# Optimization experiments

Measured on AMD Instinct MI355X. Metric: run time of the kernel, lower is better.

The kernel has to match this reference:

```python
import jax, jax.numpy as jnp
import numpy as np

B, H, W, C, F = 32, 32, 32, 256, 64
K_NEIGH = 32  # L1 pixel-distance cutoff used for the static mask


def _distance_mask(h, w, k):
    # coords: [hw, 2] of (y, x); L1 pixel distances, normalized by max(h, w)
    ys, xs = jnp.meshgrid(jnp.arange(h), jnp.arange(w), indexing='ij')
    coords = jnp.stack([ys, xs], axis=-1).reshape(-1, 2).astype(jnp.float32)
    diff = jnp.abs(coords[:, None, :] - coords[None, :, :]).sum(-1)  # [hw, hw], == cdist p=1
    dist = diff / float(max(h, w))
    return jnp.where(diff <= k, dist, 0.0)


def setup_inputs() -> dict:
    key = jax.random.key(0)
    ks = jax.random.split(key, 7)
    return {
        'feature_map': jax.random.normal(ks[0], (B, H, W, C), dtype=jnp.float32),
        'emb_W': jax.random.normal(ks[1], (F, C), dtype=jnp.float32) * (1.0 / np.sqrt(C)),
        'emb_b': jax.random.normal(ks[2], (F,), dtype=jnp.float32) * 0.01,
        'attn_W': jax.random.normal(ks[3], (C, C), dtype=jnp.float32) * (1.0 / np.sqrt(C)),
        'attn_b': jax.random.normal(ks[4], (C,), dtype=jnp.float32) * 0.01,
        'thr_W': jax.random.normal(ks[5], (1, C), dtype=jnp.float32) * (1.0 / np.sqrt(C)),
        'thr_b': jax.random.normal(ks[6], (1,), dtype=jnp.float32) * 0.01,
        'layer': 0,
    }


def reference(feature_map, emb_W, emb_b, attn_W, attn_b, thr_W, thr_b, layer):
    b, h, w, c = feature_map.shape
    hw = h * w
    x = feature_map.reshape(b, hw, c)  # row-major (y, x) flatten, matches torch view

    # 1x1 conv -> per-pixel linear: instance embeddings [b, hw, F]
    emb = jnp.einsum('bnc,fc->bnf', x, emb_W) + emb_b

    # squared Euclidean pairwise distances (cdist p=2, then squared)
    sq = jnp.sum(emb * emb, axis=-1)  # [b, hw]
    d2 = jnp.maximum(sq[:, :, None] + sq[:, None, :]
                     - 2.0 * jnp.einsum('bnf,bmf->bnm', emb, emb), 0.0)

    mask = _distance_mask(h, w, K_NEIGH)  # [hw, hw] static buffer
    sim = jax.nn.softmax(jnp.exp(-d2) - (1.0 - mask), axis=-1)  # [b, hw, hw]

    # shortcut = attention_conv(feature_map): [b, hw, c]
    shortcut = jnp.einsum('bnc,dc->bnd', x, attn_W) + attn_b

    # per-pixel learned threshold: [b, hw]
    Tinst = (jnp.einsum('bnc,oc->bno', shortcut, thr_W) + thr_b)[..., 0]

    A = jax.nn.softmax(jnp.maximum(sim - Tinst[:, None, :], 0.0), axis=-1)

    # bmm: out[b, i, c] = sum_j shortcut[b, j, c] * A[b, i, j]
    attn_out = jnp.einsum('bjc,bij->bic', shortcut, A)

    res = (x + attn_out).reshape(b, h, w, c)
    return res
```

## Files before the change

kernel.cpp:

```cpp
#include <hip/hip_runtime.h>
#include <hip/hip_bf16.h>


typedef short bf16x8 __attribute__((ext_vector_type(8)));
typedef float f32x4 __attribute__((ext_vector_type(4)));

__device__ __forceinline__ unsigned short f2bf(float f) {
  unsigned u = __float_as_uint(f);
  u += 0x7fffu + ((u >> 16) & 1u);
  return (unsigned short)(u >> 16);
}
__device__ __forceinline__ float bf2f(unsigned short h) {
  return __uint_as_float(((unsigned)h) << 16);
}
__device__ __forceinline__ unsigned pack2(float a, float b) {
  return (unsigned)f2bf(a) | ((unsigned)f2bf(b) << 16);
}
__device__ __forceinline__ f32x4 mfma16(bf16x8 a, bf16x8 b, f32x4 c) {
  return __builtin_amdgcn_mfma_f32_16x16x32_bf16(a, b, c, 0, 0, 0);
}
__device__ __forceinline__ int iabs(int v) { return v < 0 ? -v : v; }
__device__ __forceinline__ void load_lds16(const void* g, void* l) {
  __builtin_amdgcn_global_load_lds(
      (const __attribute__((address_space(1))) unsigned int*)g,
      (__attribute__((address_space(3))) unsigned int*)l, 16, 0, 0);
}

__global__ __launch_bounds__(256) void k_emb(const float* __restrict__ x,
                                             const float* __restrict__ embW,
                                             const float* __restrict__ embB,
                                             unsigned short* __restrict__ embb,
                                             float* __restrict__ sq) {
  __shared__ unsigned short xs[64][40];
  __shared__ unsigned short ws[64][40];
  __shared__ float sqls[64];
  const int t = threadIdx.x;
  const int Mbase = blockIdx.x * 64;
  const int lane = t & 63, wave = t >> 6;
  const int wm = wave >> 1, wn = wave & 1;
  const int l15 = lane & 15, quad = lane >> 4;

  f32x4 acc[2][2] = {};
  for (int k0 = 0; k0 < 256; k0 += 32) {
    {
      int row = t >> 2, c0 = (t & 3) * 8;
      const float* src = x + (size_t)(Mbase + row) * 256 + k0 + c0;
      float4 a = *(const float4*)src;
      float4 b = *(const float4*)(src + 4);
      uint4 p; p.x = pack2(a.x, a.y); p.y = pack2(a.z, a.w);
      p.z = pack2(b.x, b.y); p.w = pack2(b.z, b.w);
      *(uint4*)&xs[row][c0] = p;
    }
    if (t < 64) {
      const float* wsrc = embW + (size_t)t * 256 + k0;
      for (int s = 0; s < 4; s++) {
        float4 a = *(const float4*)(wsrc + s * 8);
        float4 b = *(const float4*)(wsrc + s * 8 + 4);
        uint4 p; p.x = pack2(a.x, a.y); p.y = pack2(a.z, a.w);
        p.z = pack2(b.x, b.y); p.w = pack2(b.z, b.w);
        *(uint4*)&ws[t][s * 8] = p;
      }
    }
    __syncthreads();
    bf16x8 af[2], bfr[2];
    for (int rt = 0; rt < 2; rt++)
      af[rt] = *(const bf16x8*)&xs[wm * 32 + rt * 16 + l15][quad * 8];
    for (int ct = 0; ct < 2; ct++)
      bfr[ct] = *(const bf16x8*)&ws[wn * 32 + ct * 16 + l15][quad * 8];
    for (int rt = 0; rt < 2; rt++)
      for (int ct = 0; ct < 2; ct++)
        acc[rt][ct] = mfma16(af[rt], bfr[ct], acc[rt][ct]);
    __syncthreads();
  }

  if (t < 64) sqls[t] = 0.f;
  __syncthreads();
  float sp[2][4] = {};
  for (int rt = 0; rt < 2; rt++)
    for (int ct = 0; ct < 2; ct++) {
      int f = wn * 32 + ct * 16 + l15;
      float bias = embB[f];
      for (int r = 0; r < 4; r++) {
        float v = acc[rt][ct][r] + bias;
        unsigned short hb = f2bf(v);
        int rowl = wm * 32 + rt * 16 + quad * 4 + r;
        embb[(size_t)(Mbase + rowl) * 64 + f] = hb;
        float vf = bf2f(hb);
        sp[rt][r] += vf * vf;
      }
    }
  for (int m = 8; m >= 1; m >>= 1)
    for (int rt = 0; rt < 2; rt++)
      for (int r = 0; r < 4; r++)
        sp[rt][r] += __shfl_xor(sp[rt][r], m);
  if (l15 == 0)
    for (int rt = 0; rt < 2; rt++)
      for (int r = 0; r < 4; r++)
        atomicAdd(&sqls[wm * 32 + rt * 16 + quad * 4 + r], sp[rt][r]);
  __syncthreads();
  if (t < 64) sq[Mbase + t] = sqls[t];
}

__global__ __launch_bounds__(256) void k_shortcut(const float* __restrict__ x,
                                                  const float* __restrict__ attnW,
                                                  const float* __restrict__ attnB,
                                                  const float* __restrict__ thrW,
                                                  const float* __restrict__ thrB,
                                                  unsigned short* __restrict__ scT,
                                                  float* __restrict__ Tout) {
  __shared__ unsigned short xs[64][40];
  __shared__ unsigned short ws[256][40];
  __shared__ unsigned short St[256][72];
  const int t = threadIdx.x;
  const int Mbase = blockIdx.x * 64;
  const int lane = t & 63, wave = t >> 6;
  const int wm = wave >> 1, wn = wave & 1;
  const int l15 = lane & 15, quad = lane >> 4;

  f32x4 acc[2][8] = {};
  for (int k0 = 0; k0 < 256; k0 += 32) {
    {
      int row = t >> 2, c0 = (t & 3) * 8;
      const float* src = x + (size_t)(Mbase + row) * 256 + k0 + c0;
      float4 a = *(const float4*)src;
      float4 b = *(const float4*)(src + 4);
      uint4 p; p.x = pack2(a.x, a.y); p.y = pack2(a.z, a.w);
      p.z = pack2(b.x, b.y); p.w = pack2(b.z, b.w);
      *(uint4*)&xs[row][c0] = p;
    }
    {
      const float* wsrc = attnW + (size_t)t * 256 + k0;
      for (int s = 0; s < 4; s++) {
        float4 a = *(const float4*)(wsrc + s * 8);
        float4 b = *(const float4*)(wsrc + s * 8 + 4);
        uint4 p; p.x = pack2(a.x, a.y); p.y = pack2(a.z, a.w);
        p.z = pack2(b.x, b.y); p.w = pack2(b.z, b.w);
        *(uint4*)&ws[t][s * 8] = p;
      }
    }
    __syncthreads();
    bf16x8 af[2];
    for (int rt = 0; rt < 2; rt++)
      af[rt] = *(const bf16x8*)&xs[wm * 32 + rt * 16 + l15][quad * 8];
    for (int nt = 0; nt < 8; nt++) {
      bf16x8 bfr = *(const bf16x8*)&ws[wn * 128 + nt * 16 + l15][quad * 8];
      for (int rt = 0; rt < 2; rt++)
        acc[rt][nt] = mfma16(af[rt], bfr, acc[rt][nt]);
    }
    __syncthreads();
  }

  for (int rt = 0; rt < 2; rt++)
    for (int nt = 0; nt < 8; nt++) {
      int c = wn * 128 + nt * 16 + l15;
      float bias = attnB[c];
      for (int r = 0; r < 4; r++) {
        float v = acc[rt][nt][r] + bias;
        int j = wm * 32 + rt * 16 + quad * 4 + r;
        St[c][j] = f2bf(v);
      }
    }
  __syncthreads();
  const int b = Mbase >> 10, jbase = Mbase & 1023;
  {
    unsigned short* dst = scT + ((size_t)b * 256 + t) * 1024 + jbase;
    for (int s = 0; s < 8; s++)
      *(uint4*)(dst + s * 8) = *(const uint4*)&St[t][s * 8];
  }
  {
    float tp = 0.f;
    int j = t >> 2, cs = (t & 3) * 64;
    for (int c = 0; c < 64; c++)
      tp += bf2f(St[cs + c][j]) * thrW[cs + c];
    tp += __shfl_xor(tp, 1);
    tp += __shfl_xor(tp, 2);
    if ((t & 3) == 0) Tout[Mbase + j] = tp + thrB[0];
  }
}

__global__ __launch_bounds__(256) void k_scores(const unsigned short* __restrict__ embb,
                                                const float* __restrict__ sq,
                                                const float* __restrict__ T,
                                                unsigned short* __restrict__ U,
                                                float* __restrict__ Z) {
  __shared__ unsigned short E_lds[16 * 1040];
  __shared__ float rbuf[16];
  const int t = threadIdx.x, lane = t & 63, wave = t >> 6;
  const int b = blockIdx.x >> 6, rb = (blockIdx.x & 63) * 16;
  const int l15 = lane & 15, quad = lane >> 4;
  const unsigned short* eb = embb + (size_t)b * 1024 * 64;

  if (t < 16) rbuf[t] = 0.f;

  const int rowA = rb + l15;
  bf16x8 a0 = *(const bf16x8*)(eb + (size_t)rowA * 64 + quad * 8);
  bf16x8 a1 = *(const bf16x8*)(eb + (size_t)rowA * 64 + 32 + quad * 8);
  const int rloc = quad * 4;
  float sqi[4]; int yi[4], xi[4];
  for (int r = 0; r < 4; r++) {
    int rowg = rb + rloc + r;
    sqi[r] = sq[b * 1024 + rowg];
    yi[r] = rowg >> 5; xi[r] = rowg & 31;
  }
  const int jq = wave * 256;
  float rp[4] = {0.f, 0.f, 0.f, 0.f};
  for (int j0 = jq; j0 < jq + 256; j0 += 16) {
    const int jr = j0 + l15;
    bf16x8 b0 = *(const bf16x8*)(eb + (size_t)jr * 64 + quad * 8);
    bf16x8 b1 = *(const bf16x8*)(eb + (size_t)jr * 64 + 32 + quad * 8);
    f32x4 g = {0.f, 0.f, 0.f, 0.f};
    g = mfma16(a0, b0, g);
    g = mfma16(a1, b1, g);
    float sqj = sq[b * 1024 + jr];
    int yj = jr >> 5, xj = jr & 31;
    for (int r = 0; r < 4; r++) {
      float d2 = fmaxf(sqi[r] + sqj - 2.f * g[r], 0.f);
      int diff = iabs(yi[r] - yj) + iabs(xi[r] - xj);
      float m = (diff <= 32) ? (float)diff * (1.f / 32.f) : 0.f;
      float s = __expf(-d2) - 1.f + m;
      unsigned short h = f2bf(__expf(s));
      E_lds[(rloc + r) * 1040 + jr] = h;
      rp[r] += bf2f(h);
    }
  }
  for (int m = 8; m >= 1; m >>= 1)
    for (int r = 0; r < 4; r++)
      rp[r] += __shfl_xor(rp[r], m);
  __syncthreads();
  if (l15 == 0)
    for (int r = 0; r < 4; r++)
      atomicAdd(&rbuf[rloc + r], rp[r]);
  __syncthreads();

  const int prow = t >> 4, seg = t & 15;
  const float invR = 1.f / rbuf[prow];
  const float* Tb = T + b * 1024;
  unsigned short* ur = U + ((size_t)(b * 1024 + rb + prow)) * 1024;
  float z = 0.f;
  for (int c = 0; c < 8; c++) {
    int j = c * 128 + seg * 8;
    union { bf16x8 v; unsigned short s[8]; } ev;
    ev.v = *(const bf16x8*)&E_lds[prow * 1040 + j];
    float4 t0 = *(const float4*)(Tb + j);
    float4 t1 = *(const float4*)(Tb + j + 4);
    float tf[8] = {t0.x, t0.y, t0.z, t0.w, t1.x, t1.y, t1.z, t1.w};
    union { uint4 v; unsigned short s[8]; } uo;
    for (int k = 0; k < 8; k++) {
      float u = __expf(fmaxf(fmaf(bf2f(ev.s[k]), invR, -tf[k]), 0.f));
      unsigned short h = f2bf(u);
      uo.s[k] = h;
      z += bf2f(h);
    }
    *(uint4*)(ur + j) = uo.v;
  }
  z += __shfl_xor(z, 1);
  z += __shfl_xor(z, 2);
  z += __shfl_xor(z, 4);
  z += __shfl_xor(z, 8);
  if (seg == 0) Z[b * 1024 + rb + prow] = z;
}

__global__ __launch_bounds__(256) void k_out(const unsigned short* __restrict__ U,
                                             const float* __restrict__ Z,
                                             const unsigned short* __restrict__ scT,
                                             const float* __restrict__ x,
                                             float* __restrict__ out) {
  __shared__ unsigned short Ab[128 * 32];
  __shared__ unsigned short Bb[128 * 32];
  const int t = threadIdx.x, lane = t & 63, wave = t >> 6;
  const int wm = wave >> 1, wn = wave & 1;
  const int l15 = lane & 15, quad = lane >> 4;
  const int x8 = blockIdx.x & 7, s = blockIdx.x >> 3;
  const int b = x8 * 4 + (s >> 4), tile = s & 15;
  const int rb = (tile >> 1) * 128, cb = (tile & 1) * 128;

  const unsigned short* Ubase = U + (size_t)b * 1024 * 1024 + (size_t)rb * 1024;
  const unsigned short* Sbase = scT + (size_t)b * 256 * 1024 + (size_t)cb * 1024;

  int c0 = wave * 64 + lane;
  int c1 = c0 + 256;
  const int r0 = c0 >> 2, o0 = (c0 & 3) * 8;
  const int r1 = c1 >> 2, o1 = (c1 & 3) * 8;

  f32x4 acc[4][4] = {};
  for (int j0 = 0; j0 < 1024; j0 += 32) {
    load_lds16(Ubase + (size_t)r0 * 1024 + j0 + o0, Ab + c0 * 8);
    load_lds16(Ubase + (size_t)r1 * 1024 + j0 + o1, Ab + c1 * 8);
    load_lds16(Sbase + (size_t)r0 * 1024 + j0 + o0, Bb + c0 * 8);
    load_lds16(Sbase + (size_t)r1 * 1024 + j0 + o1, Bb + c1 * 8);
    __syncthreads();
    bf16x8 af[4], bf[4];
    for (int i = 0; i < 4; i++)
      af[i] = *(const bf16x8*)&Ab[(wm * 64 + i * 16 + l15) * 32 + quad * 8];
    for (int i = 0; i < 4; i++)
      bf[i] = *(const bf16x8*)&Bb[(wn * 64 + i * 16 + l15) * 32 + quad * 8];
    for (int i = 0; i < 4; i++)
      for (int j = 0; j < 4; j++)
        acc[i][j] = mfma16(af[i], bf[j], acc[i][j]);
    __syncthreads();
  }

  const int colb = cb + wn * 64;
  for (int i = 0; i < 4; i++) {
    int rowb = rb + wm * 64 + i * 16 + quad * 4;
    float iz[4];
    for (int r = 0; r < 4; r++) iz[r] = 1.f / Z[b * 1024 + rowb + r];
    for (int j = 0; j < 4; j++) {
      int c = colb + j * 16 + l15;
      for (int r = 0; r < 4; r++) {
        size_t idx = ((size_t)(b * 1024 + rowb + r)) * 256 + c;
        out[idx] = x[idx] + acc[i][j][r] * iz[r];
      }
    }
  }
}

extern "C" void kernel_launch(void* const* d_in, const int* in_sizes, int n_in,
                              void* d_out, int out_size, void* d_ws, size_t ws_size,
                              hipStream_t stream) {
  const float* x     = (const float*)d_in[0];
  const float* embW  = (const float*)d_in[1];
  const float* embB  = (const float*)d_in[2];
  const float* attnW = (const float*)d_in[3];
  const float* attnB = (const float*)d_in[4];
  const float* thrW  = (const float*)d_in[5];
  const float* thrB  = (const float*)d_in[6];
  float* out = (float*)d_out;

  char* ws = (char*)d_ws;
  unsigned short* embb = (unsigned short*)(ws);
  unsigned short* scT  = (unsigned short*)(ws + (4ull << 20));
  unsigned short* U    = (unsigned short*)(ws + (20ull << 20));
  float* sq = (float*)(ws + (84ull << 20));
  float* T  = (float*)(ws + (84ull << 20) + (128ull << 10));
  float* Z  = (float*)(ws + (84ull << 20) + (256ull << 10));

  k_emb<<<512, 256, 0, stream>>>(x, embW, embB, embb, sq);
  k_shortcut<<<512, 256, 0, stream>>>(x, attnW, attnB, thrW, thrB, scT, T);
  k_scores<<<2048, 256, 0, stream>>>(embb, sq, T, U, Z);
  k_out<<<512, 256, 0, stream>>>(U, Z, scT, x, out);
}
```

Measured before the change: 208.2 us.

## Precast inputs to bf16 in a prep kernel and tabulate mask exponent factor

Adds a prep kernel that converts x and both weight matrices to bf16 once, so k_emb and k_shortcut load bf16 directly instead of each converting fp32 per tile. It also precomputes a 63x63 table of exp(mask-1) indexed by pixel offset, which turns the score inner loop's mask arithmetic and one exp into a table lookup and a multiply. The cost is an extra launch plus an extra write and read of the bf16 copy of x, and a small change in rounding because the mask factor is stored in bf16.

```diff
diff --git a/kernel.cpp b/kernel.cpp
--- a/kernel.cpp
+++ b/kernel.cpp
@@ -12,9 +12,6 @@
 }
 __device__ __forceinline__ float bf2f(unsigned short h) {
   return __uint_as_float(((unsigned)h) << 16);
-}
-__device__ __forceinline__ unsigned pack2(float a, float b) {
-  return (unsigned)f2bf(a) | ((unsigned)f2bf(b) << 16);
 }
 __device__ __forceinline__ f32x4 mfma16(bf16x8 a, bf16x8 b, f32x4 c) {
   return __builtin_amdgcn_mfma_f32_16x16x32_bf16(a, b, c, 0, 0, 0);
@@ -26,8 +23,32 @@
       (__attribute__((address_space(3))) unsigned int*)l, 16, 0, 0);
 }
 
-__global__ __launch_bounds__(256) void k_emb(const float* __restrict__ x,
-                                             const float* __restrict__ embW,
+__global__ __launch_bounds__(256) void k_prep(const float* __restrict__ x,
+                                              const float* __restrict__ embW,
+                                              const float* __restrict__ attnW,
+                                              unsigned short* __restrict__ xb,
+                                              unsigned short* __restrict__ Wb,
+                                              unsigned short* __restrict__ Msk63) {
+  const int tid = blockIdx.x * 256 + threadIdx.x;
+  {
+    float4 v = *(const float4*)(x + (size_t)tid * 4);
+    ushort4 p; p.x = f2bf(v.x); p.y = f2bf(v.y); p.z = f2bf(v.z); p.w = f2bf(v.w);
+    *(ushort4*)(xb + (size_t)tid * 4) = p;
+  }
+  if (tid < 81920) {
+    float v = (tid < 16384) ? embW[tid] : attnW[tid - 16384];
+    Wb[tid] = f2bf(v);
+  }
+  if (tid < 3969) {
+    int dy = tid / 63 - 31, dx = tid % 63 - 31;
+    int diff = iabs(dy) + iabs(dx);
+    float m = (diff <= 32) ? (float)diff * (1.f / 32.f) : 0.f;
+    Msk63[tid] = f2bf(__expf(m - 1.f));
+  }
+}
+
+__global__ __launch_bounds__(256) void k_emb(const unsigned short* __restrict__ xb,
+                                             const unsigned short* __restrict__ Wb,
                                              const float* __restrict__ embB,
                                              unsigned short* __restrict__ embb,
                                              float* __restrict__ sq) {
@@ -44,22 +65,13 @@
   for (int k0 = 0; k0 < 256; k0 += 32) {
     {
       int row = t >> 2, c0 = (t & 3) * 8;
-      const float* src = x + (size_t)(Mbase + row) * 256 + k0 + c0;
-      float4 a = *(const float4*)src;
-      float4 b = *(const float4*)(src + 4);
-      uint4 p; p.x = pack2(a.x, a.y); p.y = pack2(a.z, a.w);
-      p.z = pack2(b.x, b.y); p.w = pack2(b.z, b.w);
-      *(uint4*)&xs[row][c0] = p;
+      *(uint4*)&xs[row][c0] =
+          *(const uint4*)(xb + (size_t)(Mbase + row) * 256 + k0 + c0);
     }
     if (t < 64) {
-      const float* wsrc = embW + (size_t)t * 256 + k0;
-      for (int s = 0; s < 4; s++) {
-        float4 a = *(const float4*)(wsrc + s * 8);
-        float4 b = *(const float4*)(wsrc + s * 8 + 4);
-        uint4 p; p.x = pack2(a.x, a.y); p.y = pack2(a.z, a.w);
-        p.z = pack2(b.x, b.y); p.w = pack2(b.z, b.w);
-        *(uint4*)&ws[t][s * 8] = p;
-      }
+      const unsigned short* wsrc = Wb + (size_t)t * 256 + k0;
+      for (int s = 0; s < 4; s++)
+        *(uint4*)&ws[t][s * 8] = *(const uint4*)(wsrc + s * 8);
     }
     __syncthreads();
     bf16x8 af[2], bfr[2];
@@ -101,8 +113,8 @@
   if (t < 64) sq[Mbase + t] = sqls[t];
 }
 
-__global__ __launch_bounds__(256) void k_shortcut(const float* __restrict__ x,
-                                                  const float* __restrict__ attnW,
+__global__ __launch_bounds__(256) void k_shortcut(const unsigned short* __restrict__ xb,
+                                                  const unsigned short* __restrict__ WbA,
                                                   const float* __restrict__ attnB,
                                                   const float* __restrict__ thrW,
                                                   const float* __restrict__ thrB,
@@ -121,22 +133,13 @@
   for (int k0 = 0; k0 < 256; k0 += 32) {
     {
       int row = t >> 2, c0 = (t & 3) * 8;
-      const float* src = x + (size_t)(Mbase + row) * 256 + k0 + c0;
-      float4 a = *(const float4*)src;
-      float4 b = *(const float4*)(src + 4);
-      uint4 p; p.x = pack2(a.x, a.y); p.y = pack2(a.z, a.w);
-      p.z = pack2(b.x, b.y); p.w = pack2(b.z, b.w);
-      *(uint4*)&xs[row][c0] = p;
+      *(uint4*)&xs[row][c0] =
+          *(const uint4*)(xb + (size_t)(Mbase + row) * 256 + k0 + c0);
     }
     {
-      const float* wsrc = attnW + (size_t)t * 256 + k0;
-      for (int s = 0; s < 4; s++) {
-        float4 a = *(const float4*)(wsrc + s * 8);
-        float4 b = *(const float4*)(wsrc + s * 8 + 4);
-        uint4 p; p.x = pack2(a.x, a.y); p.y = pack2(a.z, a.w);
-        p.z = pack2(b.x, b.y); p.w = pack2(b.z, b.w);
-        *(uint4*)&ws[t][s * 8] = p;
-      }
+      const unsigned short* wsrc = WbA + (size_t)t * 256 + k0;
+      for (int s = 0; s < 4; s++)
+        *(uint4*)&ws[t][s * 8] = *(const uint4*)(wsrc + s * 8);
     }
     __syncthreads();
     bf16x8 af[2];
@@ -181,6 +184,7 @@
 __global__ __launch_bounds__(256) void k_scores(const unsigned short* __restrict__ embb,
                                                 const float* __restrict__ sq,
                                                 const float* __restrict__ T,
+                                                const unsigned short* __restrict__ Msk63,
                                                 unsigned short* __restrict__ U,
                                                 float* __restrict__ Z) {
   __shared__ unsigned short E_lds[16 * 1040];
@@ -196,10 +200,10 @@
   bf16x8 a0 = *(const bf16x8*)(eb + (size_t)rowA * 64 + quad * 8);
   bf16x8 a1 = *(const bf16x8*)(eb + (size_t)rowA * 64 + 32 + quad * 8);
   const int rloc = quad * 4;
-  float sqi[4]; int yi[4], xi[4];
+  float nsqi[4]; int yi[4], xi[4];
   for (int r = 0; r < 4; r++) {
     int rowg = rb + rloc + r;
-    sqi[r] = sq[b * 1024 + rowg];
+    nsqi[r] = -sq[b * 1024 + rowg];
     yi[r] = rowg >> 5; xi[r] = rowg & 31;
   }
   const int jq = wave * 256;
@@ -214,11 +218,11 @@
     float sqj = sq[b * 1024 + jr];
     int yj = jr >> 5, xj = jr & 31;
     for (int r = 0; r < 4; r++) {
-      float d2 = fmaxf(sqi[r] + sqj - 2.f * g[r], 0.f);
-      int diff = iabs(yi[r] - yj) + iabs(xi[r] - xj);
-      float m = (diff <= 32) ? (float)diff * (1.f / 32.f) : 0.f;
-      float s = __expf(-d2) - 1.f + m;
-      unsigned short h = f2bf(__expf(s));
+      float w = fminf(fmaf(2.f, g[r], nsqi[r] - sqj), 0.f);
+      float v = __expf(w);
+      int idx = (yi[r] - yj) * 63 + (xi[r] - xj) + 1984;
+      float e = __expf(v) * bf2f(Msk63[idx]);
+      unsigned short h = f2bf(e);
       E_lds[(rloc + r) * 1040 + jr] = h;
       rp[r] += bf2f(h);
     }
@@ -331,12 +335,16 @@
   unsigned short* embb = (unsigned short*)(ws);
   unsigned short* scT  = (unsigned short*)(ws + (4ull << 20));
   unsigned short* U    = (unsigned short*)(ws + (20ull << 20));
+  unsigned short* xb   = (unsigned short*)(ws + (20ull << 20));
+  unsigned short* Wb   = (unsigned short*)(ws + (36ull << 20));
   float* sq = (float*)(ws + (84ull << 20));
   float* T  = (float*)(ws + (84ull << 20) + (128ull << 10));
   float* Z  = (float*)(ws + (84ull << 20) + (256ull << 10));
-
-  k_emb<<<512, 256, 0, stream>>>(x, embW, embB, embb, sq);
-  k_shortcut<<<512, 256, 0, stream>>>(x, attnW, attnB, thrW, thrB, scT, T);
-  k_scores<<<2048, 256, 0, stream>>>(embb, sq, T, U, Z);
+  unsigned short* Msk63 = (unsigned short*)(ws + (84ull << 20) + (384ull << 10));
+
+  k_prep<<<8192, 256, 0, stream>>>(x, embW, attnW, xb, Wb, Msk63);
+  k_emb<<<512, 256, 0, stream>>>(xb, Wb, embB, embb, sq);
+  k_shortcut<<<512, 256, 0, stream>>>(xb, Wb + 16384, attnB, thrW, thrB, scT, T);
+  k_scores<<<2048, 256, 0, stream>>>(embb, sq, T, Msk63, U, Z);
   k_out<<<512, 256, 0, stream>>>(U, Z, scT, x, out);
 }
```

New measurement: 205.1 us. About the same (-1.5%).
